# Performance work log

Hardware: AMD Instinct MI355X
Metric: run time of the kernel (lower is better)

The kernel has to match this reference:

```python
import jax, jax.numpy as jnp
import numpy as np

HIDDEN, KEY_DIM, VALUE_DIM = 1024, 1024, 1024
BATCH, SEQ = 8, 2048


def setup_inputs() -> dict:
    key = jax.random.key(0)
    ks = jax.random.split(key, 9)
    s = lambda fan_in: 1.0 / np.sqrt(fan_in)
    return {
        "y_all": jax.random.normal(ks[0], (BATCH, SEQ, HIDDEN), dtype=jnp.float32),
        # torch nn.Linear weights stored as (in, out) for x @ W + b
        "Wq": jax.random.uniform(ks[1], (HIDDEN, KEY_DIM), jnp.float32, -s(HIDDEN), s(HIDDEN)),
        "bq": jax.random.uniform(ks[2], (KEY_DIM,), jnp.float32, -s(HIDDEN), s(HIDDEN)),
        "Wk": jax.random.uniform(ks[3], (HIDDEN, KEY_DIM), jnp.float32, -s(HIDDEN), s(HIDDEN)),
        "bk": jax.random.uniform(ks[4], (KEY_DIM,), jnp.float32, -s(HIDDEN), s(HIDDEN)),
        "Wv": jax.random.uniform(ks[5], (HIDDEN, VALUE_DIM), jnp.float32, -s(HIDDEN), s(HIDDEN)),
        "bv": jax.random.uniform(ks[6], (VALUE_DIM,), jnp.float32, -s(HIDDEN), s(HIDDEN)),
        "Wo": jax.random.uniform(ks[7], (VALUE_DIM, HIDDEN), jnp.float32, -s(VALUE_DIM), s(VALUE_DIM)),
        "bo": jax.random.uniform(ks[8], (HIDDEN,), jnp.float32, -s(VALUE_DIM), s(VALUE_DIM)),
    }


def reference(y_all, Wq, bq, Wk, bk, Wv, bv, Wo, bo):
    # Original loops over t, each step attending last hidden state to the full
    # prefix. Equivalent to a single causal-masked attention pass.
    B, T, H = y_all.shape
    dk = Wq.shape[1]
    q = (y_all @ Wq + bq) / jnp.sqrt(jnp.asarray(dk, y_all.dtype))  # [B,T,dk]
    k = y_all @ Wk + bk                                              # [B,T,dk]
    v = y_all @ Wv + bv                                              # [B,T,dv]
    scores = jnp.einsum("bid,bjd->bij", q, k)                        # [B,T,T]
    causal = jnp.tril(jnp.ones((T, T), dtype=bool))                  # j <= i
    scores = jnp.where(causal, scores, -jnp.inf)
    weights = jax.nn.softmax(scores, axis=-1)
    ctx = jnp.einsum("bij,bjd->bid", weights, v)                     # [B,T,dv]
    return ctx @ Wo + bo                                             # [B,T,H]
```

## Files before the change

kernel.cpp:

```cpp
#include <hip/hip_runtime.h>

typedef __attribute__((ext_vector_type(8))) __bf16 bf16x8;
typedef __attribute__((ext_vector_type(4))) float f32x4;
typedef __attribute__((ext_vector_type(4))) float f4;
typedef __attribute__((ext_vector_type(4))) unsigned short ushort4_t;

__device__ inline void gload16(const void* g, void* l) {
  __builtin_amdgcn_global_load_lds(
      (const __attribute__((address_space(1))) unsigned int*)g,
      (__attribute__((address_space(3))) unsigned int*)l, 16, 0, 0);
}

__global__ void convert_bf16_k(const float* __restrict__ in, __bf16* __restrict__ out, int n8) {
  int i = blockIdx.x * blockDim.x + threadIdx.x;
  int stride = gridDim.x * blockDim.x;
  for (; i < n8; i += stride) {
    f4 a = ((const f4*)in)[2 * (long long)i];
    f4 b = ((const f4*)in)[2 * (long long)i + 1];
    bf16x8 o;
#pragma unroll
    for (int e = 0; e < 4; e++) { o[e] = (__bf16)a[e]; o[e + 4] = (__bf16)b[e]; }
    ((bf16x8*)out)[i] = o;
  }
}

__global__ void pack_bias_k(const float* __restrict__ bq, const float* __restrict__ bk,
                            const float* __restrict__ bv, float* __restrict__ out) {
  int i = blockIdx.x * 256 + threadIdx.x;
  if (i >= 3072) return;
  const float* src = (i < 1024) ? bq : (i < 2048) ? bk : bv;
  out[i] = src[i & 1023];
}

__global__ void transpose_w_k(const float* __restrict__ W0, const float* __restrict__ W1,
                              const float* __restrict__ W2, const float* __restrict__ W3,
                              __bf16* __restrict__ out) {
  int z = blockIdx.z;
  const float* W = (z == 0) ? W0 : (z == 1) ? W1 : (z == 2) ? W2 : W3;
  __bf16* O = out + (long long)z * 1048576;
  __shared__ float tile[32][33];
  int tx = threadIdx.x, ty = threadIdx.y;
  int n0 = blockIdx.x * 32, k0 = blockIdx.y * 32;
#pragma unroll
  for (int i = 0; i < 4; i++)
    tile[ty + i * 8][tx] = W[(long long)(k0 + ty + i * 8) * 1024 + n0 + tx];
  __syncthreads();
#pragma unroll
  for (int i = 0; i < 4; i++)
    O[(long long)(n0 + ty + i * 8) * 1024 + k0 + tx] = (__bf16)tile[tx][ty + i * 8];
}

#define FENCE asm volatile("" ::: "memory")


#define LOADA(BASE, MIB)                                                       \
  _Pragma("unroll") for (int mi = 0; mi < 4; mi++)                             \
      _Pragma("unroll") for (int kh = 0; kh < 2; kh++) {                       \
    int row = ((MIB) + mi) * 16 + ln15;                                        \
    int pb = (row * 128 + (kh * 32 + kq * 8) * 2) ^ ((row & 7) << 4);          \
    a[mi][kh] = *(const bf16x8*)((BASE) + pb);                                 \
  }

#define LOADB(BASE, NIB)                                                       \
  _Pragma("unroll") for (int ni = 0; ni < 2; ni++)                             \
      _Pragma("unroll") for (int kh = 0; kh < 2; kh++) {                       \
    int row = brow0 + ((NIB) + ni) * 16 + ln15;                                \
    int pb = (row * 128 + (kh * 32 + kq * 8) * 2) ^ ((row & 7) << 4);          \
    b[(NIB) + ni][kh] = *(const bf16x8*)((BASE) + pb);                         \
  }

#define MFMAQ(MI0, NI0)                                                        \
  _Pragma("unroll") for (int mi = 0; mi < 4; mi++)                             \
      _Pragma("unroll") for (int ni = 0; ni < 2; ni++)                         \
          _Pragma("unroll") for (int kh = 0; kh < 2; kh++)                     \
              acc[(MI0) + mi][(NI0) + ni] =                                    \
      __builtin_amdgcn_mfma_f32_16x16x32_bf16(a[mi][kh], b[(NI0) + ni][kh],    \
                                              acc[(MI0) + mi][(NI0) + ni], 0, 0, 0);

#define BARW                                           \
  FENCE;                                               \
  __builtin_amdgcn_s_barrier();                        \
  FENCE;                                               \
  __builtin_amdgcn_s_setprio(1);

#define ENDP                                           \
  __builtin_amdgcn_s_setprio(0);                       \
  FENCE;                                               \
  __builtin_amdgcn_s_barrier();                        \
  FENCE;

#define ENDPB                                          \
  __builtin_amdgcn_s_setprio(0);                       \
  asm volatile("s_waitcnt vmcnt(8)" ::: "memory");     \
  __builtin_amdgcn_s_barrier();                        \
  FENCE;

template <int OUT, int SWZ>
__global__ __launch_bounds__(512, 2) void gemm8(
    const __bf16* __restrict__ A0, int lda, long long sAz,
    const __bf16* __restrict__ B0, int ldb, long long sBz,
    void* __restrict__ C0v, int ldc, long long sCz,
    const float* __restrict__ bias0, int sBiasZ,
    float scale_z0, int k_tiles_base, int k_tiles_per_br,
    __bf16* __restrict__ vt_out) {
  int br, bc, z;
  {
    const int lin = (blockIdx.z * gridDim.y + blockIdx.y) * gridDim.x + blockIdx.x;
    if (SWZ == 1) {
      const int q = lin & 7, c = lin >> 3;
      br = q * 8 + (c & 7);
      const int rest = c >> 3;
      const int nby = gridDim.y;
      bc = rest % nby;
      z = rest / nby;
    } else if (SWZ == 2) {
      const int q = lin & 7, c = lin >> 3;
      z = q;
      int b0 = (int)((sqrtf((float)(8 * c + 1)) - 1.0f) * 0.5f);
      int c0 = c - ((b0 * (b0 + 1)) >> 1);
      if (c0 < 0) { b0--; c0 = c - ((b0 * (b0 + 1)) >> 1); }
      if (c0 > b0) { b0++; c0 = c - ((b0 * (b0 + 1)) >> 1); }
      br = b0;
      bc = c0;
    } else if (SWZ == 3) {
      const int q = lin & 7, c = lin >> 3;
      z = q;
      br = c & 7;
      bc = c >> 3;
    } else {
      const int nbx = gridDim.x, nby = gridDim.y;
      const int nwg = nbx * nby * gridDim.z;
      const int cpx = nwg >> 3;
      const int swz = (lin & 7) * cpx + (lin >> 3);
      br = swz % nbx;
      const int tmp = swz / nbx;
      bc = tmp % nby;
      z = tmp / nby;
    }
  }
  const int kt = k_tiles_base + k_tiles_per_br * br;

  __shared__ __align__(16) __bf16 lds[81920];

  const int t = threadIdx.x, w = t >> 6, lane = t & 63;
  const int wm = w >> 2, wn = w & 3;
  const int ln15 = lane & 15, kq = lane >> 4;
  const int bh = wn >> 1, brow0 = (wn & 1) * 64;

  const __bf16* A = A0 + (long long)z * sAz + (long long)br * 256 * lda;
  const __bf16* B = B0 + (long long)z * sBz + (long long)bc * 256 * ldb;

  int r0s[2], c0s[2];
#pragma unroll
  for (int i = 0; i < 2; i++) {
    int o = i * 8192 + t * 16;
    int lo = o ^ (((o >> 7) & 7) << 4);
    r0s[i] = lo >> 7;
    c0s[i] = (lo & 127) >> 1;
  }
  const __bf16 *sA0[2], *sA1[2], *sB0[2], *sB1[2];
#pragma unroll
  for (int i = 0; i < 2; i++) {
    sA0[i] = A + (long long)r0s[i] * lda + c0s[i];
    sA1[i] = A + (long long)(r0s[i] + 128) * lda + c0s[i];
    sB0[i] = B + (long long)r0s[i] * ldb + c0s[i];
    sB1[i] = B + (long long)(r0s[i] + 128) * ldb + c0s[i];
  }

  auto stg = [&](const __bf16* const* src, __bf16* lbase, int g) {
    int kc = g < kt ? g : kt - 1;
#pragma unroll
    for (int i = 0; i < 2; i++)
      gload16(src[i] + kc * 64, lbase + i * 4096 + w * 512);
  };

  f32x4 acc[8][4] = {};
  bf16x8 a[4][2], b[4][2];

  stg(sA0, lds, 0);
  stg(sA1, lds + 8192, 0);
  stg(sB0, lds + 49152, 0);
  stg(sB1, lds + 49152 + 8192, 0);
  stg(sA0, lds + 16384, 1);
  stg(sA1, lds + 16384 + 8192, 1);
  stg(sB0, lds + 65536, 1);
  stg(sB1, lds + 65536 + 8192, 1);
  asm volatile("s_waitcnt vmcnt(8)" ::: "memory");
  __builtin_amdgcn_s_barrier();
  FENCE;

  int ap = 0, ad = 2;
  for (int kk = 0; kk < kt; kk++) {
    __bf16* Ab = lds + ap * 16384;
    __bf16* Bb = lds + 49152 + (kk & 1) * 16384;
    __bf16* Ad = lds + ad * 16384;
    __bf16* Bd = Bb;
    const char* Aw = (const char*)(Ab + wm * 8192);
    const char* Bw = (const char*)(Bb + bh * 8192);
    LOADA(Aw, 0) LOADB(Bw, 0)
    stg(sA0, Ad, kk + 2);
    BARW MFMAQ(0, 0) ENDP
    LOADB(Bw, 2)
    stg(sA1, Ad + 8192, kk + 2);
    BARW MFMAQ(0, 2) ENDP
    LOADA(Aw, 4)
    stg(sB0, Bd, kk + 2);
    BARW MFMAQ(4, 2) ENDP
    stg(sB1, Bd + 8192, kk + 2);
    BARW MFMAQ(4, 0) ENDPB
    ap = (ap == 2) ? 0 : ap + 1;
    ad = (ad == 2) ? 0 : ad + 1;
  }

  {
    const int row0 = br * 256 + wm * 128 + kq * 4;
    const int col0 = bc * 256 + wn * 64 + ln15;
    const float scale = (z == 0) ? scale_z0 : 1.0f;
    const float* bias = bias0 ? (bias0 + (long long)z * sBiasZ) : nullptr;
#pragma unroll
    for (int mi = 0; mi < 8; mi++) {
#pragma unroll
      for (int ni = 0; ni < 4; ni++) {
        const int rr = row0 + mi * 16;
        const int cc = col0 + ni * 16;
        const float bb = bias ? bias[cc] : 0.0f;
#pragma unroll
        for (int j = 0; j < 4; j++) {
          float v = (acc[mi][ni][j] + bb) * scale;
          long long off = (long long)z * sCz + (long long)(rr + j) * ldc + cc;
          if (OUT == 1)
            ((float*)C0v)[off] = v;
          else
            ((__bf16*)C0v)[off] = (__bf16)v;
        }
      }
    }
  }
  (void)vt_out;
}

template <int OUT, int SWZ>
__global__ __launch_bounds__(512, 4) void gemm2w(
    const __bf16* __restrict__ A0, int lda, long long sAz,
    const __bf16* __restrict__ B0, int ldb, long long sBz,
    void* __restrict__ C0v, int ldc, long long sCz,
    const float* __restrict__ bias0, int sBiasZ,
    float scale_z0, int k_tiles_base, int k_tiles_per_br,
    __bf16* __restrict__ vt_out) {
  int br, bc, z;
  {
    const int lin = (blockIdx.z * gridDim.y + blockIdx.y) * gridDim.x + blockIdx.x;
    if (SWZ == 4) {
      z = lin & 7;
      const int r = (lin >> 3) & 7;
      bc = (lin >> 6) & 3;
      const int half = lin >> 8;
      br = half ? (7 - r) : (8 + r);
    } else {
      const int q = lin & 7, c = lin >> 3;
      br = q * 16 + (c & 15);
      const int rest = c >> 4;
      const int nby = gridDim.y;
      bc = rest % nby;
      z = rest / nby;
    }
  }
  const int kt = k_tiles_base + k_tiles_per_br * br;

  __shared__ __align__(16) __bf16 lds[36864];

  const int t = threadIdx.x, w = t >> 6, lane = t & 63;
  const int wm = w >> 2, wn = w & 3;
  const int ln15 = lane & 15, kq = lane >> 4;

  const __bf16* A = A0 + (long long)z * sAz + (long long)br * 128 * lda;
  const __bf16* B = B0 + (long long)z * sBz + (long long)bc * 256 * ldb;

  const __bf16* sA;
  const __bf16* sB[2];
  {
    int o = t * 16;
    int lo = o ^ (((o >> 7) & 3) << 4);
    sA = A + (long long)(lo >> 6) * lda + ((lo & 63) >> 1);
  }
#pragma unroll
  for (int i = 0; i < 2; i++) {
    int o = i * 8192 + t * 16;
    int lo = o ^ (((o >> 7) & 3) << 4);
    sB[i] = B + (long long)(lo >> 6) * ldb + ((lo & 63) >> 1);
  }

  auto stgA = [&](int buf, int g) {
    int kc = g < kt ? g : kt - 1;
    gload16(sA + kc * 32, lds + buf * 4096 + w * 512);
  };
  auto stgB = [&](int buf, int g) {
    int kc = g < kt ? g : kt - 1;
#pragma unroll
    for (int i = 0; i < 2; i++)
      gload16(sB[i] + kc * 32, lds + 12288 + buf * 8192 + i * 4096 + w * 512);
  };

  f32x4 acc[4][4] = {};
  bf16x8 a[4], b[4];

  stgA(0, 0); stgB(0, 0);
  stgA(1, 1); stgB(1, 1);
  asm volatile("s_waitcnt vmcnt(3)" ::: "memory");
  __builtin_amdgcn_s_barrier();
  FENCE;

  int cb = 0, db = 2;
  for (int kk = 0; kk < kt; kk++) {
    const char* Ab = (const char*)(lds + cb * 4096);
    const char* Bb = (const char*)(lds + 12288 + cb * 8192);
#pragma unroll
    for (int mi = 0; mi < 4; mi++) {
      int row = wm * 64 + mi * 16 + ln15;
      int pb = (row * 64 + kq * 16) ^ (((row >> 1) & 3) << 4);
      a[mi] = *(const bf16x8*)(Ab + pb);
    }
#pragma unroll
    for (int ni = 0; ni < 4; ni++) {
      int row = wn * 64 + ni * 16 + ln15;
      int pb = (row * 64 + kq * 16) ^ (((row >> 1) & 3) << 4);
      b[ni] = *(const bf16x8*)(Bb + pb);
    }
    stgA(db, kk + 2);
    stgB(db, kk + 2);
    FENCE;
    __builtin_amdgcn_s_barrier();
    FENCE;
    __builtin_amdgcn_s_setprio(1);
#pragma unroll
    for (int mi = 0; mi < 4; mi++)
#pragma unroll
      for (int ni = 0; ni < 4; ni++)
        acc[mi][ni] = __builtin_amdgcn_mfma_f32_16x16x32_bf16(
            a[mi], b[ni], acc[mi][ni], 0, 0, 0);
    __builtin_amdgcn_s_setprio(0);
    asm volatile("s_waitcnt vmcnt(3)" ::: "memory");
    __builtin_amdgcn_s_barrier();
    FENCE;
    cb = (cb == 2) ? 0 : cb + 1;
    db = (db == 2) ? 0 : db + 1;
  }
  asm volatile("s_waitcnt vmcnt(0)" ::: "memory");

  if (OUT == 2 && z == 2) {
    __syncthreads();
    char* lb = (char*)lds;
#pragma unroll
    for (int mi = 0; mi < 4; mi++) {
#pragma unroll
      for (int ni = 0; ni < 4; ni++) {
        const int d = wn * 64 + ni * 16 + ln15;
        const int tl = wm * 64 + kq * 4 + mi * 16;
        const float bb = bias0[2048 + bc * 256 + d];
        ushort4_t p;
#pragma unroll
        for (int j = 0; j < 4; j++) {
          union { __bf16 h; unsigned short u; } cv;
          cv.h = (__bf16)(acc[mi][ni][j] + bb);
          p[j] = cv.u;
        }
        int byte = (d * 256 + tl * 2) ^ ((d & 7) << 4);
        *(ushort4_t*)(lb + byte) = p;
      }
    }
    __syncthreads();
    const int bz = br >> 4;
    const int t0 = (br & 15) * 128;
    __bf16* vbase = vt_out + (long long)bz * 2097152 +
                    (long long)(bc * 256) * 2048 + t0;
#pragma unroll
    for (int it = 0; it < 8; it++) {
      int idx = it * 512 + t;
      int d = idx >> 4, tc = idx & 15;
      int byte = (d * 256 + tc * 16) ^ ((d & 7) << 4);
      bf16x8 vv = *(const bf16x8*)(lb + byte);
      *(bf16x8*)(vbase + (long long)d * 2048 + tc * 8) = vv;
    }
  } else {
    const int row0 = br * 128 + wm * 64 + kq * 4;
    const int col0 = bc * 256 + wn * 64 + ln15;
    const float scale = (z == 0) ? scale_z0 : 1.0f;
    const float* bias = bias0 ? (bias0 + (long long)z * sBiasZ) : nullptr;
#pragma unroll
    for (int mi = 0; mi < 4; mi++) {
#pragma unroll
      for (int ni = 0; ni < 4; ni++) {
        const int rr = row0 + mi * 16;
        const int cc = col0 + ni * 16;
        const float bb = bias ? bias[cc] : 0.0f;
#pragma unroll
        for (int j = 0; j < 4; j++) {
          float v = (acc[mi][ni][j] + bb) * scale;
          long long off = (long long)z * sCz + (long long)(rr + j) * ldc + cc;
          if (OUT == 1)
            ((float*)C0v)[off] = v;
          else
            ((__bf16*)C0v)[off] = (__bf16)v;
        }
      }
    }
  }
}

__global__ __launch_bounds__(256) void softmax_rows(__bf16* __restrict__ S) {
  const int row = blockIdx.x;
  const int i = row & 2047;
  __bf16* s = S + (long long)row * 2048;
  const int Lpad = (i + 256) & ~255;
  const int t = threadIdx.x;
  const int j0 = t * 8;
  const int wid = t >> 6, lane = t & 63;
  const bool active = j0 < Lpad;

  float v[8];
  float mymax = -3.0e38f;
  if (active) {
    bf16x8 x = *(const bf16x8*)(s + j0);
#pragma unroll
    for (int e = 0; e < 8; e++) {
      float f = (float)x[e];
      v[e] = ((j0 + e) <= i) ? f : -3.0e38f;
      mymax = fmaxf(mymax, v[e]);
    }
  }
  float mw = mymax;
#pragma unroll
  for (int o = 32; o >= 1; o >>= 1) mw = fmaxf(mw, __shfl_xor(mw, o));
  __shared__ float redm[4];
  __shared__ float reds[4];
  if (lane == 0) redm[wid] = mw;
  __syncthreads();
  const float m = fmaxf(fmaxf(redm[0], redm[1]), fmaxf(redm[2], redm[3]));

  float e8[8];
  float mysum = 0.0f;
  if (active) {
#pragma unroll
    for (int e = 0; e < 8; e++) {
      float ev = ((j0 + e) <= i) ? __expf(v[e] - m) : 0.0f;
      e8[e] = ev;
      mysum += ev;
    }
  } else {
#pragma unroll
    for (int e = 0; e < 8; e++) e8[e] = 0.0f;
  }
  float sw = mysum;
#pragma unroll
  for (int o = 32; o >= 1; o >>= 1) sw += __shfl_xor(sw, o);
  if (lane == 0) reds[wid] = sw;
  __syncthreads();
  const float l = reds[0] + reds[1] + reds[2] + reds[3];
  const float rl = 1.0f / l;
  if (active) {
    bf16x8 o;
#pragma unroll
    for (int e = 0; e < 8; e++) o[e] = (__bf16)(e8[e] * rl);
    *(bf16x8*)(s + j0) = o;
  }
}

extern "C" void kernel_launch(void* const* d_in, const int* in_sizes, int n_in,
                              void* d_out, int out_size, void* d_ws, size_t ws_size,
                              hipStream_t stream) {
  const float* y  = (const float*)d_in[0];
  const float* Wq = (const float*)d_in[1];
  const float* bq = (const float*)d_in[2];
  const float* Wk = (const float*)d_in[3];
  const float* bk = (const float*)d_in[4];
  const float* Wv = (const float*)d_in[5];
  const float* bv = (const float*)d_in[6];
  const float* Wo = (const float*)d_in[7];
  const float* bo = (const float*)d_in[8];

  char* ws = (char*)d_ws;
  __bf16* Xb   = (__bf16*)(ws + 0);
  __bf16* Wt   = (__bf16*)(ws + 33554432);
  float*  bqkv = (float*)(ws + 41943040);
  __bf16* Qb   = (__bf16*)(ws + 41955328);
  __bf16* Kb   = (__bf16*)(ws + 75509760);
  __bf16* Vt   = (__bf16*)(ws + 109064192);
  __bf16* Sb   = (__bf16*)(ws + 142618624);
  __bf16* ctx  = (__bf16*)(ws + 0);

  if (ws_size < 209727488u) return;

  convert_bf16_k<<<2048, 256, 0, stream>>>(y, Xb, 2097152);
  pack_bias_k<<<12, 256, 0, stream>>>(bq, bk, bv, bqkv);
  transpose_w_k<<<dim3(32, 32, 4), dim3(32, 8), 0, stream>>>(Wq, Wk, Wv, Wo, Wt);

  gemm2w<2, 0><<<dim3(128, 4, 3), 512, 0, stream>>>(
      Xb, 1024, 0LL, Wt, 1024, 1048576LL,
      Qb, 1024, 16777216LL, bqkv, 1024, 0.03125f, 32, 0, Vt);

  gemm8<0, 2><<<dim3(36, 1, 8), 512, 0, stream>>>(
      Qb, 1024, 2097152LL, Kb, 1024, 2097152LL,
      Sb, 2048, 4194304LL, nullptr, 0, 1.0f, 16, 0, nullptr);

  softmax_rows<<<16384, 256, 0, stream>>>(Sb);

  gemm2w<0, 4><<<dim3(512, 1, 1), 512, 0, stream>>>(
      Sb, 2048, 4194304LL, Vt, 2048, 2097152LL,
      ctx, 1024, 2097152LL, nullptr, 0, 1.0f, 4, 4, nullptr);

  gemm8<1, 1><<<dim3(64, 4, 1), 512, 0, stream>>>(
      ctx, 1024, 0LL, Wt + 3 * 1048576, 1024, 0LL,
      d_out, 1024, 0LL, bo, 0, 1.0f, 16, 0, nullptr);
}
```

Measured before the change: 315.2 us.

## Merge prep kernels and tile causal QK^T with finer triangular gemm2w blocks

Fuses the bf16 conversion, weight transpose and bias packing into a single prep kernel to cut launch overhead. The causal QK^T score GEMM moves from the 256-row gemm8 triangular tiling to gemm2w with a new triangular swizzle over 128-row tiles, which skips more masked work and gives finer load balance. Softmax padding is narrowed from 256 to 128 to match the new tile granularity. The smaller tiles trade some data reuse per block for less wasted compute above the diagonal.

```diff
diff --git a/kernel.cpp b/kernel.cpp
--- a/kernel.cpp
+++ b/kernel.cpp
@@ -11,46 +11,49 @@
       (__attribute__((address_space(3))) unsigned int*)l, 16, 0, 0);
 }
 
-__global__ void convert_bf16_k(const float* __restrict__ in, __bf16* __restrict__ out, int n8) {
-  int i = blockIdx.x * blockDim.x + threadIdx.x;
-  int stride = gridDim.x * blockDim.x;
-  for (; i < n8; i += stride) {
-    f4 a = ((const f4*)in)[2 * (long long)i];
-    f4 b = ((const f4*)in)[2 * (long long)i + 1];
-    bf16x8 o;
-#pragma unroll
-    for (int e = 0; e < 4; e++) { o[e] = (__bf16)a[e]; o[e + 4] = (__bf16)b[e]; }
-    ((bf16x8*)out)[i] = o;
+#define FENCE asm volatile("" ::: "memory")
+
+__global__ __launch_bounds__(256) void prep_k(
+    const float* __restrict__ y,
+    const float* __restrict__ Wq, const float* __restrict__ Wk,
+    const float* __restrict__ Wv, const float* __restrict__ Wo,
+    const float* __restrict__ bq, const float* __restrict__ bk,
+    const float* __restrict__ bv,
+    __bf16* __restrict__ Xb, __bf16* __restrict__ Wt, float* __restrict__ bqkv) {
+  __shared__ float tile[32][33];
+  const int bid = blockIdx.x, t = threadIdx.x;
+  if (bid < 2048) {
+    for (int i = bid * 256 + t; i < 2097152; i += 524288) {
+      f4 a = ((const f4*)y)[2 * (long long)i];
+      f4 b = ((const f4*)y)[2 * (long long)i + 1];
+      bf16x8 o;
+#pragma unroll
+      for (int e = 0; e < 4; e++) { o[e] = (__bf16)a[e]; o[e + 4] = (__bf16)b[e]; }
+      ((bf16x8*)Xb)[i] = o;
+    }
+  } else if (bid < 6144) {
+    const int idx = bid - 2048;
+    const int z = idx >> 10, rem = idx & 1023;
+    const int bx = rem & 31, by = rem >> 5;
+    const float* W = (z == 0) ? Wq : (z == 1) ? Wk : (z == 2) ? Wv : Wo;
+    __bf16* O = Wt + (long long)z * 1048576;
+    const int tx = t & 31, ty = t >> 5;
+    const int n0 = bx * 32, k0 = by * 32;
+#pragma unroll
+    for (int i = 0; i < 4; i++)
+      tile[ty + i * 8][tx] = W[(long long)(k0 + ty + i * 8) * 1024 + n0 + tx];
+    __syncthreads();
+#pragma unroll
+    for (int i = 0; i < 4; i++)
+      O[(long long)(n0 + ty + i * 8) * 1024 + k0 + tx] = (__bf16)tile[tx][ty + i * 8];
+  } else {
+    const int i = (bid - 6144) * 256 + t;
+    if (i < 3072) {
+      const float* src = (i < 1024) ? bq : (i < 2048) ? bk : bv;
+      bqkv[i] = src[i & 1023];
+    }
   }
 }
-
-__global__ void pack_bias_k(const float* __restrict__ bq, const float* __restrict__ bk,
-                            const float* __restrict__ bv, float* __restrict__ out) {
-  int i = blockIdx.x * 256 + threadIdx.x;
-  if (i >= 3072) return;
-  const float* src = (i < 1024) ? bq : (i < 2048) ? bk : bv;
-  out[i] = src[i & 1023];
-}
-
-__global__ void transpose_w_k(const float* __restrict__ W0, const float* __restrict__ W1,
-                              const float* __restrict__ W2, const float* __restrict__ W3,
-                              __bf16* __restrict__ out) {
-  int z = blockIdx.z;
-  const float* W = (z == 0) ? W0 : (z == 1) ? W1 : (z == 2) ? W2 : W3;
-  __bf16* O = out + (long long)z * 1048576;
-  __shared__ float tile[32][33];
-  int tx = threadIdx.x, ty = threadIdx.y;
-  int n0 = blockIdx.x * 32, k0 = blockIdx.y * 32;
-#pragma unroll
-  for (int i = 0; i < 4; i++)
-    tile[ty + i * 8][tx] = W[(long long)(k0 + ty + i * 8) * 1024 + n0 + tx];
-  __syncthreads();
-#pragma unroll
-  for (int i = 0; i < 4; i++)
-    O[(long long)(n0 + ty + i * 8) * 1024 + k0 + tx] = (__bf16)tile[tx][ty + i * 8];
-}
-
-#define FENCE asm volatile("" ::: "memory")
 
 
 #define LOADA(BASE, MIB)                                                       \
@@ -101,8 +104,7 @@
     const __bf16* __restrict__ B0, int ldb, long long sBz,
     void* __restrict__ C0v, int ldc, long long sCz,
     const float* __restrict__ bias0, int sBiasZ,
-    float scale_z0, int k_tiles_base, int k_tiles_per_br,
-    __bf16* __restrict__ vt_out) {
+    float scale_z0, int k_tiles_base, int k_tiles_per_br) {
   int br, bc, z;
   {
     const int lin = (blockIdx.z * gridDim.y + blockIdx.y) * gridDim.x + blockIdx.x;
@@ -113,20 +115,6 @@
       const int nby = gridDim.y;
       bc = rest % nby;
       z = rest / nby;
-    } else if (SWZ == 2) {
-      const int q = lin & 7, c = lin >> 3;
-      z = q;
-      int b0 = (int)((sqrtf((float)(8 * c + 1)) - 1.0f) * 0.5f);
-      int c0 = c - ((b0 * (b0 + 1)) >> 1);
-      if (c0 < 0) { b0--; c0 = c - ((b0 * (b0 + 1)) >> 1); }
-      if (c0 > b0) { b0++; c0 = c - ((b0 * (b0 + 1)) >> 1); }
-      br = b0;
-      bc = c0;
-    } else if (SWZ == 3) {
-      const int q = lin & 7, c = lin >> 3;
-      z = q;
-      br = c & 7;
-      bc = c >> 3;
     } else {
       const int nbx = gridDim.x, nby = gridDim.y;
       const int nwg = nbx * nby * gridDim.z;
@@ -236,7 +224,6 @@
       }
     }
   }
-  (void)vt_out;
 }
 
 template <int OUT, int SWZ>
@@ -256,6 +243,15 @@
       bc = (lin >> 6) & 3;
       const int half = lin >> 8;
       br = half ? (7 - r) : (8 + r);
+    } else if (SWZ == 5) {
+      z = lin & 7;
+      const int c = lin >> 3;
+      int m = (int)((sqrtf((float)(4 * c + 1)) - 1.0f) * 0.5f);
+      if (c < m * (m + 1)) m--;
+      if (c >= (m + 1) * (m + 2)) m++;
+      const int r = c - m * (m + 1);
+      if (r >= m + 1) { br = 2 * m + 1; bc = r - (m + 1); }
+      else { br = 2 * m; bc = r; }
     } else {
       const int q = lin & 7, c = lin >> 3;
       br = q * 16 + (c & 15);
@@ -411,7 +407,7 @@
   const int row = blockIdx.x;
   const int i = row & 2047;
   __bf16* s = S + (long long)row * 2048;
-  const int Lpad = (i + 256) & ~255;
+  const int Lpad = (i + 128) & ~127;
   const int t = threadIdx.x;
   const int j0 = t * 8;
   const int wid = t >> 6, lane = t & 63;
@@ -490,17 +486,15 @@
 
   if (ws_size < 209727488u) return;
 
-  convert_bf16_k<<<2048, 256, 0, stream>>>(y, Xb, 2097152);
-  pack_bias_k<<<12, 256, 0, stream>>>(bq, bk, bv, bqkv);
-  transpose_w_k<<<dim3(32, 32, 4), dim3(32, 8), 0, stream>>>(Wq, Wk, Wv, Wo, Wt);
+  prep_k<<<6156, 256, 0, stream>>>(y, Wq, Wk, Wv, Wo, bq, bk, bv, Xb, Wt, bqkv);
 
   gemm2w<2, 0><<<dim3(128, 4, 3), 512, 0, stream>>>(
       Xb, 1024, 0LL, Wt, 1024, 1048576LL,
       Qb, 1024, 16777216LL, bqkv, 1024, 0.03125f, 32, 0, Vt);
 
-  gemm8<0, 2><<<dim3(36, 1, 8), 512, 0, stream>>>(
+  gemm2w<0, 5><<<dim3(576, 1, 1), 512, 0, stream>>>(
       Qb, 1024, 2097152LL, Kb, 1024, 2097152LL,
-      Sb, 2048, 4194304LL, nullptr, 0, 1.0f, 16, 0, nullptr);
+      Sb, 2048, 4194304LL, nullptr, 0, 1.0f, 32, 0, nullptr);
 
   softmax_rows<<<16384, 256, 0, stream>>>(Sb);
 
@@ -510,5 +504,5 @@
 
   gemm8<1, 1><<<dim3(64, 4, 1), 512, 0, stream>>>(
       ctx, 1024, 0LL, Wt + 3 * 1048576, 1024, 0LL,
-      d_out, 1024, 0LL, bo, 0, 1.0f, 16, 0, nullptr);
+      d_out, 1024, 0LL, bo, 0, 1.0f, 16, 0);
 }
```

After: 298.6 us. -5.3%, faster.
